# Performance work log

Measured on AMD Instinct MI355X. Metric: run time of the kernel, lower is better.

The kernel has to match this reference:

```python
import jax, jax.numpy as jnp
import numpy as np

# Config (matches init_kwargs): range [-32,32]^3, voxel 0.5 -> 128^3 grid; BEV 200x200
PC_LOW = np.array([-32.0, -32.0, -32.0], dtype=np.float32)
PC_HIGH = np.array([32.0, 32.0, 32.0], dtype=np.float32)
VOX = 0.5
G = 128
BEV_H, BEV_W = 200, 200
BN_EPS = 1e-5
STRIDES = [1, 2, 1, 2, 1, 1]


def setup_inputs() -> dict:
    key = jax.random.key(0)
    ks = jax.random.split(key, 10)
    N = 2_000_000
    xyz = jax.random.uniform(ks[0], (N, 3), jnp.float32, minval=-32.0, maxval=32.0)
    inten = jax.random.uniform(ks[1], (N, 1), jnp.float32)
    points = jnp.concatenate([xyz, inten], axis=1)  # (N,4)
    chans = [(32, 4), (64, 32), (64, 64), (128, 64), (128, 128), (256, 128)]
    inp = {"points": points}
    for i, (co, ci) in enumerate(chans):
        fan_in = ci * 27
        inp[f"w{i+1}"] = jax.random.normal(ks[2 + i], (co, ci, 3, 3, 3), jnp.float32) / np.sqrt(fan_in)
        inp[f"g{i+1}"] = jnp.ones((co,), jnp.float32)
        inp[f"b{i+1}"] = jnp.zeros((co,), jnp.float32)
    return inp


def _voxelize(points):
    # range filtering + floor-binning + clamp, faithful to voxelize_points (dense path: scatter-ADD)
    low = jnp.asarray(PC_LOW)
    high = jnp.asarray(PC_HIGH)
    mask = jnp.all((points[:, :3] >= low) & (points[:, :3] <= high), axis=1)
    coords = jnp.floor((points[:, :3] - low) / VOX).astype(jnp.int32)
    coords = jnp.clip(coords, 0, G - 1)
    vals = points * mask[:, None].astype(points.dtype)  # invalid points contribute 0
    # original indexes voxel_grid[:, z, y, x]
    grid = jnp.zeros((G, G, G, 4), points.dtype)
    grid = grid.at[coords[:, 2], coords[:, 1], coords[:, 0]].add(vals)
    return jnp.transpose(grid, (3, 0, 1, 2))  # (4, G, G, G)


def _conv3d(x, w, s):
    # PyTorch Conv3d(k=3, padding=1, stride=s), NCDHW
    return jax.lax.conv_general_dilated(
        x, w, window_strides=(s, s, s), padding=[(1, 1), (1, 1), (1, 1)],
        dimension_numbers=("NCDHW", "OIDHW", "NCDHW"))


def _bn_relu(x, g, b):
    # eval-mode BN: running_mean=0, running_var=1
    scale = (g / jnp.sqrt(1.0 + BN_EPS))[None, :, None, None, None]
    return jax.nn.relu(x * scale + b[None, :, None, None, None])


def reference(points, w1, w2, w3, w4, w5, w6,
              g1, g2, g3, g4, g5, g6,
              b1, b2, b3, b4, b5, b6):
    ws = [w1, w2, w3, w4, w5, w6]
    gs = [g1, g2, g3, g4, g5, g6]
    bs = [b1, b2, b3, b4, b5, b6]
    x = _voxelize(points)[None]  # (1,4,G,G,G)
    for w, g, b, s in zip(ws, gs, bs, STRIDES):
        x = _bn_relu(_conv3d(x, w, s), g, b)
    feat = x[0]  # (256, G/4, G/4, G/4)
    bev = jnp.max(feat, axis=2)  # torch.max(..., dim=2) on (C,D1,D2,D3) -> (C,D1,D3)
    # F.interpolate bilinear align_corners=False == jax.image.resize half-pixel bilinear
    bev = jax.image.resize(bev, (bev.shape[0], BEV_H, BEV_W), method="bilinear")
    return bev
```

## Files before the change

### kernel.cpp

```cpp
#include <hip/hip_runtime.h>
#include <hip/hip_fp16.h>
#include <cstdint>
#include <cstddef>

typedef __attribute__((ext_vector_type(8))) short short8;
typedef __attribute__((ext_vector_type(8))) _Float16 half8;
typedef __attribute__((ext_vector_type(16))) float f32x16;

__device__ __forceinline__ float bf2f(unsigned short u) { return __uint_as_float(((unsigned)u) << 16); }
__device__ __forceinline__ unsigned short f2bf(float f) {
    unsigned u = __float_as_uint(f);
    return (unsigned short)((u + 0x7fffu + ((u >> 16) & 1u)) >> 16);
}
__device__ __forceinline__ void sync_lds() {
    asm volatile("s_waitcnt lgkmcnt(0)\n\ts_barrier" ::: "memory");
}

static constexpr float BN_INV = 0.9999950000374997f;


__device__ __forceinline__ int vox_bucket(float4 p, bool& ok) {
    ok = !(p.x < -32.f || p.x > 32.f || p.y < -32.f || p.y > 32.f || p.z < -32.f || p.z > 32.f);
    int cy = min(max((int)floorf((p.y + 32.f) * 2.f), 0), 127);
    int cz = min(max((int)floorf((p.z + 32.f) * 2.f), 0), 127);
    return cz * 4 + (cy >> 5);
}

__global__ __launch_bounds__(256) void vox_count(const float4* __restrict__ pts,
                                                 int* __restrict__ cnt, int N) {
    __shared__ int h[512];
    for (int t = threadIdx.x; t < 512; t += 256) h[t] = 0;
    __syncthreads();
    int stride = gridDim.x * 256;
    for (int i = blockIdx.x * 256 + threadIdx.x; i < N; i += stride) {
        float4 p = pts[i];
        bool ok;
        int bk = vox_bucket(p, ok);
        if (ok) atomicAdd(&h[bk], 1);
    }
    __syncthreads();
    for (int t = threadIdx.x; t < 512; t += 256)
        if (h[t]) atomicAdd(&cnt[t], h[t]);
}

__global__ void vox_scan(const int* __restrict__ cnt, int* __restrict__ off,
                         int* __restrict__ cur) {
    __shared__ int c[512];
    int t = threadIdx.x;
    c[t] = cnt[t];
    __syncthreads();
    int s = 0;
    for (int i = 0; i < t; ++i) s += c[i];
    off[t] = s;
    cur[t] = s;
}

__global__ __launch_bounds__(256) void vox_scatter(const float4* __restrict__ pts,
                                                   int* __restrict__ cur,
                                                   float4* __restrict__ sorted, int N) {
    __shared__ int h[512];
    __shared__ int base[512];
    int b0 = blockIdx.x * 4096;
    for (int t = threadIdx.x; t < 512; t += 256) h[t] = 0;
    __syncthreads();
    float4 p[16];
    int bk[16];
#pragma unroll
    for (int j = 0; j < 16; ++j) {
        int i = b0 + j * 256 + threadIdx.x;
        bk[j] = -1;
        if (i < N) {
            p[j] = pts[i];
            bool ok;
            int b = vox_bucket(p[j], ok);
            if (ok) {
                bk[j] = b;
                atomicAdd(&h[b], 1);
            }
        }
    }
    __syncthreads();
    for (int t = threadIdx.x; t < 512; t += 256) {
        int n = h[t];
        base[t] = n ? atomicAdd(&cur[t], n) : 0;
        h[t] = 0;
    }
    __syncthreads();
#pragma unroll
    for (int j = 0; j < 16; ++j) {
        if (bk[j] >= 0) {
            int r = atomicAdd(&h[bk[j]], 1);
            sorted[base[bk[j]] + r] = p[j];
        }
    }
}

__global__ __launch_bounds__(256) void vox_accum(const float4* __restrict__ sorted,
                                                 const int* __restrict__ off,
                                                 const int* __restrict__ cnt,
                                                 __half2* __restrict__ grid) {
    __shared__ float s[32 * 128 * 4];
    for (int t = threadIdx.x; t < 16384; t += 256) s[t] = 0.f;
    __syncthreads();
    int bid = blockIdx.x;
    int bz = bid >> 2;
    int ylo = (bid & 3) << 5;
    int b = off[bid], n = cnt[bid];
    for (int i = threadIdx.x; i < n; i += 256) {
        float4 p = sorted[b + i];
        int cx = min(max((int)floorf((p.x + 32.f) * 2.f), 0), 127);
        int cy = min(max((int)floorf((p.y + 32.f) * 2.f), 0), 127);
        float* v = s + ((cy - ylo) * 128 + cx) * 4;
        unsafeAtomicAdd(v + 0, p.x);
        unsafeAtomicAdd(v + 1, p.y);
        unsafeAtomicAdd(v + 2, p.z);
        unsafeAtomicAdd(v + 3, p.w);
    }
    __syncthreads();
    for (int t = threadIdx.x; t < 4096; t += 256) {
        int ry = t >> 7, cx = t & 127;
        const float* v = s + t * 4;
        union { __half2 h[2]; float2 f; } u;
        u.h[0] = __floats2half2_rn(v[0], v[1]);
        u.h[1] = __floats2half2_rn(v[2], v[3]);
        int gi = (((bz + 1) * 130 + (ylo + ry + 1)) * 130 + (cx + 1)) * 2;
        *(float2*)(grid + gi) = u.f;
    }
}

__global__ __launch_bounds__(256) void pad_zero(unsigned short* __restrict__ buf,
                                                int Xp, int Zp, int C) {
    const int cpc = (C >= 8) ? (C / 8) : 1;
    long i = (long)blockIdx.x * 256 + threadIdx.x;
    long nz = (long)2 * Xp * Xp;
    long ny = (long)(Zp - 2) * 2 * Xp;
    long nx = (long)(Zp - 2) * (Xp - 2) * 2;
    long total = (nz + ny + nx) * cpc;
    if (i >= total) return;
    long cell = i / cpc;
    int ch = (int)(i - cell * cpc) * 8;
    int z, y, x;
    if (cell < nz) {
        long r = cell;
        z = (r >= (long)Xp * Xp) ? (Zp - 1) : 0;
        r %= (long)Xp * Xp;
        y = (int)(r / Xp);
        x = (int)(r % Xp);
    } else if (cell < nz + ny) {
        long r = cell - nz;
        z = 1 + (int)(r / (2 * Xp));
        int s = (int)(r % (2 * Xp));
        y = (s >= Xp) ? (Xp - 1) : 0;
        x = (s >= Xp) ? (s - Xp) : s;
    } else {
        long r = cell - nz - ny;
        z = 1 + (int)(r / ((Xp - 2) * 2));
        int s = (int)(r % ((Xp - 2) * 2));
        y = 1 + (s >> 1);
        x = (s & 1) ? (Xp - 1) : 0;
    }
    unsigned short* p = buf + (((long)z * Xp + y) * Xp + x) * C + ch;
    if (C >= 8) {
        *(short8*)p = (short8){0, 0, 0, 0, 0, 0, 0, 0};
    } else {
        *(float2*)p = (float2){0.f, 0.f};
    }
}
static inline int pad_blocks(int Xp, int Zp, int C) {
    long cells = (long)2 * Xp * Xp + (long)(Zp - 2) * 2 * Xp + (long)(Zp - 2) * (Xp - 2) * 2;
    long thr = cells * ((C >= 8) ? (C / 8) : 1);
    return (int)((thr + 255) / 256);
}

__global__ __launch_bounds__(256) void repack_w(const float* __restrict__ w, const float* __restrict__ g,
                                                unsigned short* __restrict__ o, int Co, int CI) {
    int i = blockIdx.x * 256 + threadIdx.x;
    int total = 27 * Co * CI;
    if (i >= total) return;
    int ci = i % CI;
    int t = i / CI;
    int co = t % Co;
    int k = t / Co;
    float v = w[((size_t)(co * CI + ci)) * 27 + k] * g[co] * BN_INV;
    o[i] = f2bf(v);
}
__global__ __launch_bounds__(256) void repack_w1m(const float* __restrict__ w, const float* __restrict__ g,
                                                  unsigned short* __restrict__ o) {
    int i = blockIdx.x * 256 + threadIdx.x;
    if (i >= 9 * 32 * 16) return;
    int k16 = i & 15;
    int co = (i >> 4) & 31;
    int p = i >> 9;
    float v = 0.f;
    if (k16 < 12) {
        int dx = k16 >> 2, ci = k16 & 3;
        int dz = p / 3, dy = p % 3;
        v = w[(co * 4 + ci) * 27 + dz * 9 + dy * 3 + dx] * g[co] * BN_INV;
    }
    o[i] = __half_as_ushort(__float2half(v));
}

__global__ __launch_bounds__(256) void conv1_mfma(
    const unsigned short* __restrict__ in, const unsigned short* __restrict__ wa,
    const float* __restrict__ beta, unsigned short* __restrict__ out,
    int zstart, int r0) {
    const int tid = threadIdx.x;
    const int l31 = tid & 31;
    const int lh = (tid >> 5) & 1;
    const int wv = tid >> 6;
    int v = blockIdx.x * 128 + wv * 32 + l31;
    int x = v & 127;
    int y = (v >> 7) & 127;
    int z = zstart + (v >> 14);

    const unsigned short* base = in + ((z * 130 + y) * 130 + x) * 4 + lh * 8;
    uint2 d0[9], d1[9];
    half8 a[9];
#pragma unroll
    for (int p = 0; p < 9; ++p) {
        int dz = p / 3, dy = p % 3;
        const unsigned short* rp = base + (dz * 130 + dy) * 520;
        d0[p] = *(const uint2*)(rp);
        d1[p] = *(const uint2*)(rp + 4);
        a[p] = *(const half8*)(wa + (p * 32 + l31) * 16 + lh * 8);
    }
    f32x16 acc = {0.f};
#pragma unroll
    for (int p = 0; p < 9; ++p) {
        uint4 braw = {d0[p].x, d0[p].y, d1[p].x, d1[p].y};
        half8 b = *(half8*)&braw;
        acc = __builtin_amdgcn_mfma_f32_32x32x16_f16(a[p], b, acc, 0, 0, 0);
    }
    int r = z - zstart + r0;
    int ob = ((r * 130 + (y + 1)) * 130 + (x + 1)) * 32;
#pragma unroll
    for (int g = 0; g < 4; ++g) {
        int cb = 4 * lh + 8 * g;
        float4 bt = *(const float4*)(beta + cb);
        ushort4 u;
        u.x = f2bf(fmaxf(acc[g * 4 + 0] + bt.x, 0.f));
        u.y = f2bf(fmaxf(acc[g * 4 + 1] + bt.y, 0.f));
        u.z = f2bf(fmaxf(acc[g * 4 + 2] + bt.z, 0.f));
        u.w = f2bf(fmaxf(acc[g * 4 + 3] + bt.w, 0.f));
        *(ushort4*)(out + ob + cb) = u;
    }
}

template <int CI, int KC, int S>
__global__ __launch_bounds__(256) void conv_mfma(
    const unsigned short* __restrict__ in, const unsigned short* __restrict__ wb,
    const float* __restrict__ beta, unsigned short* __restrict__ out,
    int D, int lgD, int Xp, int Xpo, int Co, int zin_base, int v_off) {

    constexpr int KCp = KC + 8;
    constexpr int OPB = KC / 8;
    constexpr int NB = KC / 16;
    constexpr int NA = KC / 32;
    constexpr int NCH = KC / 16;
    constexpr int NCC = CI / KC;
    constexpr int STOT = 27 * NCC;

    __shared__ __align__(16) short sA[2 * 64 * KCp];
    __shared__ __align__(16) short sB[2 * 128 * KCp];

    const int tid = threadIdx.x;
    const int l31 = tid & 31;
    const int lh = (tid >> 5) & 1;
    const int wv = tid >> 6;

    const unsigned gx = gridDim.x;
    const unsigned lin = blockIdx.y * gx + blockIdx.x;
    const unsigned q = (gx * gridDim.y) >> 3;
    const unsigned lin2 = (lin & 7) * q + (lin >> 3);
    const unsigned bxs = lin2 % gx;
    const unsigned bys = lin2 / gx;
    const int co0 = bxs * 64;

    int bgIdx[NB], blB[NB];
#pragma unroll
    for (int j = 0; j < NB; ++j) {
        int idx = tid + j * 256;
        int vL = idx / OPB;
        int oct = idx - vL * OPB;
        int vg = v_off + bys * 128 + vL;
        int x = vg & (D - 1);
        int ry = vg >> lgD;
        int y = ry & (D - 1);
        int z = ry >> lgD;
        bgIdx[j] = ((z * S * Xp + y * S) * Xp + x * S) * CI + oct * 8;
        blB[j] = vL * KCp + oct * 8;
    }
    int agIdx[NA], alA[NA];
#pragma unroll
    for (int j = 0; j < NA; ++j) {
        int idx = tid + j * 256;
        int cA = idx / OPB;
        int oct = idx - cA * OPB;
        agIdx[j] = (co0 + cA) * CI + oct * 8;
        alA[j] = cA * KCp + oct * 8;
    }
    const int bfr = (wv * 32 + l31) * KCp + lh * 8;
    const int afr = l31 * KCp + lh * 8;

    short8 rB[2][NB], rA[2][NA];

    auto loadStage = [&](int s, int r) {
        int k = s / NCC;
        int c0 = (s - k * NCC) * KC;
        int dz = k / 9;
        int rr = k - dz * 9;
        int dy = rr / 3;
        int dx = rr - dy * 3;
        int kb = (((dz - zin_base) * Xp + dy) * Xp + dx) * CI + c0;
        int ka = k * Co * CI + c0;
#pragma unroll
        for (int j = 0; j < NB; ++j) rB[r][j] = *(const short8*)(in + bgIdx[j] + kb);
#pragma unroll
        for (int j = 0; j < NA; ++j) rA[r][j] = *(const short8*)(wb + agIdx[j] + ka);
    };
    auto storeLDS = [&](int r, int buf) {
#pragma unroll
        for (int j = 0; j < NB; ++j) *(short8*)(sB + buf * 128 * KCp + blB[j]) = rB[r][j];
#pragma unroll
        for (int j = 0; j < NA; ++j) *(short8*)(sA + buf * 64 * KCp + alA[j]) = rA[r][j];
    };

    f32x16 acc0 = {0.f}, acc1 = {0.f};

    loadStage(0, 0);
    loadStage(1, 1);
    storeLDS(0, 0);
    sync_lds();

#pragma unroll
    for (int s = 0; s < STOT; ++s) {
        if (s + 2 < STOT) loadStage(s + 2, s & 1);
        const short* pB = sB + (s & 1) * 128 * KCp + bfr;
        const short* pA = sA + (s & 1) * 64 * KCp + afr;
#pragma unroll
        for (int c = 0; c < NCH; ++c) {
            short8 bv = *(const short8*)(pB + c * 16);
            short8 a0 = *(const short8*)(pA + c * 16);
            short8 a1 = *(const short8*)(pA + 32 * KCp + c * 16);
            acc0 = __builtin_amdgcn_mfma_f32_32x32x16_bf16(a0, bv, acc0, 0, 0, 0);
            acc1 = __builtin_amdgcn_mfma_f32_32x32x16_bf16(a1, bv, acc1, 0, 0, 0);
        }
        if (s + 1 < STOT) {
            storeLDS((s + 1) & 1, (s + 1) & 1);
            sync_lds();
        }
    }

    int vg = v_off + bys * 128 + wv * 32 + l31;
    int x = vg & (D - 1);
    int ry = vg >> lgD;
    int y = ry & (D - 1);
    int z = ry >> lgD;
    size_t ob = (((size_t)(z + 1) * Xpo + (y + 1)) * Xpo + (x + 1)) * Co + co0;
#pragma unroll
    for (int cot = 0; cot < 2; ++cot) {
        const f32x16& a = cot ? acc1 : acc0;
#pragma unroll
        for (int g = 0; g < 4; ++g) {
            int cb = cot * 32 + 4 * lh + 8 * g;
            float4 bt = *(const float4*)(beta + co0 + cb);
            ushort4 u;
            u.x = f2bf(fmaxf(a[g * 4 + 0] + bt.x, 0.f));
            u.y = f2bf(fmaxf(a[g * 4 + 1] + bt.y, 0.f));
            u.z = f2bf(fmaxf(a[g * 4 + 2] + bt.z, 0.f));
            u.w = f2bf(fmaxf(a[g * 4 + 3] + bt.w, 0.f));
            *(ushort4*)(out + ob + cb) = u;
        }
    }
}

template <int CI, int S>
__global__ __launch_bounds__(256, 2) void conv_mfma_w(
    const unsigned short* __restrict__ in, const unsigned short* __restrict__ wb,
    const float* __restrict__ beta, unsigned short* __restrict__ out,
    int D, int lgD, int Xp, int Xpo, int Co, int zin_base, int v_off) {

    constexpr int KC = 64;
    constexpr int KCp = KC + 8;
    constexpr int OPB = KC / 8;
    constexpr int NB = 4;
    constexpr int NA = 4;
    constexpr int NCH = 4;
    constexpr int NCC = CI / KC;
    constexpr int STOT = 27 * NCC;

    __shared__ __align__(16) short sA[2 * 128 * KCp];
    __shared__ __align__(16) short sB[2 * 128 * KCp];

    const int tid = threadIdx.x;
    const int l31 = tid & 31;
    const int lh = (tid >> 5) & 1;
    const int wv = tid >> 6;
    const int wr = wv >> 1;
    const int wc = wv & 1;

    const unsigned gx = gridDim.x;
    const unsigned lin = blockIdx.y * gx + blockIdx.x;
    const unsigned q = (gx * gridDim.y) >> 3;
    const unsigned lin2 = (lin & 7) * q + (lin >> 3);
    const unsigned bxs = lin2 % gx;
    const unsigned bys = lin2 / gx;
    const int co0 = bxs * 128;

    int bgIdx[NB], blB[NB];
#pragma unroll
    for (int j = 0; j < NB; ++j) {
        int idx = tid + j * 256;
        int vL = idx / OPB;
        int oct = idx - vL * OPB;
        int vg = v_off + bys * 128 + vL;
        int x = vg & (D - 1);
        int ry = vg >> lgD;
        int y = ry & (D - 1);
        int z = ry >> lgD;
        bgIdx[j] = ((z * S * Xp + y * S) * Xp + x * S) * CI + oct * 8;
        blB[j] = vL * KCp + oct * 8;
    }
    int agIdx[NA], alA[NA];
#pragma unroll
    for (int j = 0; j < NA; ++j) {
        int idx = tid + j * 256;
        int cA = idx / OPB;
        int oct = idx - cA * OPB;
        agIdx[j] = (co0 + cA) * CI + oct * 8;
        alA[j] = cA * KCp + oct * 8;
    }
    const int bfr = (wc * 64 + l31) * KCp + lh * 8;
    const int afr = (wr * 64 + l31) * KCp + lh * 8;

    short8 rB[2][NB], rA[2][NA];

    auto loadStage = [&](int s, int r) {
        int k = s / NCC;
        int c0 = (s - k * NCC) * KC;
        int dz = k / 9;
        int rr = k - dz * 9;
        int dy = rr / 3;
        int dx = rr - dy * 3;
        int kb = (((dz - zin_base) * Xp + dy) * Xp + dx) * CI + c0;
        int ka = k * Co * CI + c0;
#pragma unroll
        for (int j = 0; j < NB; ++j) rB[r][j] = *(const short8*)(in + bgIdx[j] + kb);
#pragma unroll
        for (int j = 0; j < NA; ++j) rA[r][j] = *(const short8*)(wb + agIdx[j] + ka);
    };
    auto storeLDS = [&](int r, int buf) {
#pragma unroll
        for (int j = 0; j < NB; ++j) *(short8*)(sB + buf * 128 * KCp + blB[j]) = rB[r][j];
#pragma unroll
        for (int j = 0; j < NA; ++j) *(short8*)(sA + buf * 128 * KCp + alA[j]) = rA[r][j];
    };

    f32x16 acc00 = {0.f}, acc01 = {0.f}, acc10 = {0.f}, acc11 = {0.f};

    loadStage(0, 0);
    loadStage(1, 1);
    storeLDS(0, 0);
    sync_lds();

#pragma unroll
    for (int s = 0; s < STOT; ++s) {
        if (s + 2 < STOT) loadStage(s + 2, s & 1);
        const short* pB = sB + (s & 1) * 128 * KCp + bfr;
        const short* pA = sA + (s & 1) * 128 * KCp + afr;
#pragma unroll
        for (int c = 0; c < NCH; ++c) {
            short8 b0 = *(const short8*)(pB + c * 16);
            short8 b1 = *(const short8*)(pB + 32 * KCp + c * 16);
            short8 a0 = *(const short8*)(pA + c * 16);
            short8 a1 = *(const short8*)(pA + 32 * KCp + c * 16);
            acc00 = __builtin_amdgcn_mfma_f32_32x32x16_bf16(a0, b0, acc00, 0, 0, 0);
            acc01 = __builtin_amdgcn_mfma_f32_32x32x16_bf16(a0, b1, acc01, 0, 0, 0);
            acc10 = __builtin_amdgcn_mfma_f32_32x32x16_bf16(a1, b0, acc10, 0, 0, 0);
            acc11 = __builtin_amdgcn_mfma_f32_32x32x16_bf16(a1, b1, acc11, 0, 0, 0);
        }
        if (s + 1 < STOT) {
            storeLDS((s + 1) & 1, (s + 1) & 1);
            sync_lds();
        }
    }

#pragma unroll
    for (int i = 0; i < 2; ++i) {
#pragma unroll
        for (int j = 0; j < 2; ++j) {
            const f32x16& a = (i == 0) ? (j == 0 ? acc00 : acc01) : (j == 0 ? acc10 : acc11);
            int vg2 = v_off + bys * 128 + wc * 64 + j * 32 + l31;
            int x = vg2 & (D - 1);
            int ry = vg2 >> lgD;
            int y = ry & (D - 1);
            int z = ry >> lgD;
            int cbase = co0 + wr * 64 + i * 32;
            size_t ob = (((size_t)(z + 1) * Xpo + (y + 1)) * Xpo + (x + 1)) * Co + cbase;
#pragma unroll
            for (int g = 0; g < 4; ++g) {
                int cb = 4 * lh + 8 * g;
                float4 bt = *(const float4*)(beta + cbase + cb);
                ushort4 u;
                u.x = f2bf(fmaxf(a[g * 4 + 0] + bt.x, 0.f));
                u.y = f2bf(fmaxf(a[g * 4 + 1] + bt.y, 0.f));
                u.z = f2bf(fmaxf(a[g * 4 + 2] + bt.z, 0.f));
                u.w = f2bf(fmaxf(a[g * 4 + 3] + bt.w, 0.f));
                *(ushort4*)(out + ob + cb) = u;
            }
        }
    }
}

__global__ __launch_bounds__(256) void bev_max_kernel(const unsigned short* __restrict__ feat,
                                                      float* __restrict__ bev) {
    int z = blockIdx.x >> 5;
    int x = blockIdx.x & 31;
    int c = threadIdx.x;
    const unsigned short* p = feat + ((((z + 1) * 34) + 1) * 34 + (x + 1)) * 256 + c;
    float mx = 0.f;
#pragma unroll
    for (int y = 0; y < 32; ++y) mx = fmaxf(mx, bf2f(p[y * 34 * 256]));
    bev[(z * 32 + x) * 256 + c] = mx;
}

__global__ __launch_bounds__(256) void resize_kernel(const float* __restrict__ bev,
                                                     float* __restrict__ out) {
    int i = blockIdx.x * 256 + threadIdx.x;
    if (i >= 256 * 200 * 200) return;
    int ox = i % 200;
    int t = i / 200;
    int oy = t % 200;
    int c = t / 200;
    const float sc = 32.0f / 200.0f;
    float fy = (oy + 0.5f) * sc - 0.5f;
    float fx = (ox + 0.5f) * sc - 0.5f;
    float fy0 = floorf(fy), fx0 = floorf(fx);
    float ty = fy - fy0, tx = fx - fx0;
    int y0 = min(max((int)fy0, 0), 31), y1 = min(max((int)fy0 + 1, 0), 31);
    int x0 = min(max((int)fx0, 0), 31), x1 = min(max((int)fx0 + 1, 0), 31);
    float v00 = bev[(y0 * 32 + x0) * 256 + c], v01 = bev[(y0 * 32 + x1) * 256 + c];
    float v10 = bev[(y1 * 32 + x0) * 256 + c], v11 = bev[(y1 * 32 + x1) * 256 + c];
    float top = v00 + tx * (v01 - v00);
    float bot = v10 + tx * (v11 - v10);
    out[i] = top + ty * (bot - top);
}

extern "C" void kernel_launch(void* const* d_in, const int* in_sizes, int n_in,
                              void* d_out, int out_size, void* d_ws, size_t ws_size,
                              hipStream_t stream) {
    const float* points = (const float*)d_in[0];
    int N = in_sizes[0] / 4;
    const float *W[6], *G[6], *B[6];
    for (int i = 0; i < 6; ++i) {
        W[i] = (const float*)d_in[1 + 3 * i];
        G[i] = (const float*)d_in[2 + 3 * i];
        B[i] = (const float*)d_in[3 + 3 * i];
    }

    char* ws = (char*)d_ws;
    const size_t MiB = 1ull << 20;
    unsigned short* gridH = (unsigned short*)(ws);
    int* cnt = (int*)(ws + 17580032);
    int* off = cnt + 512;
    int* cur = off + 512;
    float4* sorted = (float4*)(ws + 18 * MiB);
    unsigned short* O1s = (unsigned short*)(ws + 18 * MiB);
    unsigned short* O2p = (unsigned short*)(ws + 104 * MiB);
    unsigned short* O3p = (unsigned short*)(ws);
    unsigned short* O4p = (unsigned short*)(ws + 37 * MiB);
    unsigned short* O5p = (unsigned short*)(ws + 48 * MiB);
    unsigned short* O6p = (unsigned short*)(ws + 59 * MiB);
    float* bev = (float*)(ws + 80 * MiB);
    unsigned short* wc1 = (unsigned short*)(ws + 140 * MiB);
    unsigned short* wb2 = (unsigned short*)(ws + 140 * MiB + 16384);
    unsigned short* wb3 = wb2 + 27 * 64 * 32;
    unsigned short* wb4 = wb3 + 27 * 64 * 64;
    unsigned short* wb5 = wb4 + 27 * 128 * 64;
    unsigned short* wb6 = wb5 + 27 * 128 * 128;

    repack_w1m<<<18, 256, 0, stream>>>(W[0], G[0], wc1);
    repack_w<<<216, 256, 0, stream>>>(W[1], G[1], wb2, 64, 32);
    repack_w<<<432, 256, 0, stream>>>(W[2], G[2], wb3, 64, 64);
    repack_w<<<864, 256, 0, stream>>>(W[3], G[3], wb4, 128, 64);
    repack_w<<<1728, 256, 0, stream>>>(W[4], G[4], wb5, 128, 128);
    repack_w<<<3456, 256, 0, stream>>>(W[5], G[5], wb6, 256, 128);

    pad_zero<<<pad_blocks(130, 130, 4), 256, 0, stream>>>(gridH, 130, 130, 4);
    hipMemsetAsync(cnt, 0, 2048, stream);
    pad_zero<<<pad_blocks(66, 66, 64), 256, 0, stream>>>(O2p, 66, 66, 64);
    vox_count<<<1024, 256, 0, stream>>>((const float4*)points, cnt, N);
    vox_scan<<<1, 512, 0, stream>>>(cnt, off, cur);
    vox_scatter<<<(N + 4095) / 4096, 256, 0, stream>>>((const float4*)points, cur, sorted, N);
    vox_accum<<<512, 256, 0, stream>>>(sorted, off, cnt, (__half2*)gridH);

    pad_zero<<<pad_blocks(130, 65, 32), 256, 0, stream>>>(O1s, 130, 65, 32);
    conv1_mfma<<<8192, 256, 0, stream>>>(gridH, wc1, B[0], O1s, 0, 1);
    conv_mfma<32, 32, 2><<<dim3(1, 1024), 256, 0, stream>>>(O1s, wb2, B[1], O2p, 64, 6, 130, 66, 64, 0, 0);
    conv1_mfma<<<8320, 256, 0, stream>>>(gridH, wc1, B[0], O1s, 63, 0);
    conv_mfma<32, 32, 2><<<dim3(1, 1024), 256, 0, stream>>>(O1s, wb2, B[1], O2p, 64, 6, 130, 66, 64, 64, 131072);

    pad_zero<<<pad_blocks(66, 66, 64), 256, 0, stream>>>(O3p, 66, 66, 64);
    pad_zero<<<pad_blocks(34, 34, 128), 256, 0, stream>>>(O4p, 34, 34, 128);
    pad_zero<<<pad_blocks(34, 34, 128), 256, 0, stream>>>(O5p, 34, 34, 128);
    pad_zero<<<pad_blocks(34, 34, 256), 256, 0, stream>>>(O6p, 34, 34, 256);

    conv_mfma<64, 64, 1><<<dim3(1, 2048), 256, 0, stream>>>(O2p, wb3, B[2], O3p, 64, 6, 66, 66, 64, 0, 0);
    conv_mfma_w<64, 2><<<dim3(1, 256), 256, 0, stream>>>(O3p, wb4, B[3], O4p, 32, 5, 66, 34, 128, 0, 0);
    conv_mfma_w<128, 1><<<dim3(1, 256), 256, 0, stream>>>(O4p, wb5, B[4], O5p, 32, 5, 34, 34, 128, 0, 0);
    conv_mfma_w<128, 1><<<dim3(2, 256), 256, 0, stream>>>(O5p, wb6, B[5], O6p, 32, 5, 34, 34, 256, 0, 0);

    bev_max_kernel<<<1024, 256, 0, stream>>>(O6p, bev);
    resize_kernel<<<40000, 256, 0, stream>>>(bev, (float*)d_out);
}
```

Measured before the change: 628.8 us.

## Enlarge conv2/conv3 tiles to 256 voxels with 2x2 MFMA register blocking

Replaces the generic conv_mfma kernel used for layers 2 and 3 with conv_mfma_p. Each block now covers 256 output voxels by 64 channels, and each wave computes a 2x2 grid of 32x32 MFMA tiles, so every LDS fragment is reused twice and fewer blocks are launched. The K chunk is fixed at 32, LDS rows are paired into 72-element padded rows to reduce bank conflicts, and launch bounds request 3 blocks per SM. The cost is more accumulator registers, and for conv3 the stage loop is only partially unrolled, giving more stages per weight load.

```diff
diff --git a/kernel.cpp b/kernel.cpp
--- a/kernel.cpp
+++ b/kernel.cpp
@@ -246,22 +246,19 @@
     }
 }
 
-template <int CI, int KC, int S>
-__global__ __launch_bounds__(256) void conv_mfma(
+template <int CI, int S>
+__global__ __launch_bounds__(256, 3) void conv_mfma_p(
     const unsigned short* __restrict__ in, const unsigned short* __restrict__ wb,
     const float* __restrict__ beta, unsigned short* __restrict__ out,
     int D, int lgD, int Xp, int Xpo, int Co, int zin_base, int v_off) {
 
-    constexpr int KCp = KC + 8;
-    constexpr int OPB = KC / 8;
-    constexpr int NB = KC / 16;
-    constexpr int NA = KC / 32;
-    constexpr int NCH = KC / 16;
+    constexpr int KC = 32;
     constexpr int NCC = CI / KC;
     constexpr int STOT = 27 * NCC;
-
-    __shared__ __align__(16) short sA[2 * 64 * KCp];
-    __shared__ __align__(16) short sB[2 * 128 * KCp];
+    constexpr int PR = 72;
+
+    __shared__ __align__(16) short sB[2 * 128 * PR];
+    __shared__ __align__(16) short sA[2 * 32 * PR];
 
     const int tid = threadIdx.x;
     const int l31 = tid & 31;
@@ -276,33 +273,33 @@
     const unsigned bys = lin2 / gx;
     const int co0 = bxs * 64;
 
-    int bgIdx[NB], blB[NB];
-#pragma unroll
-    for (int j = 0; j < NB; ++j) {
+    int bgIdx[4], blB[4];
+#pragma unroll
+    for (int j = 0; j < 4; ++j) {
         int idx = tid + j * 256;
-        int vL = idx / OPB;
-        int oct = idx - vL * OPB;
-        int vg = v_off + bys * 128 + vL;
+        int vL = idx >> 2;
+        int oct = idx & 3;
+        int vg = v_off + bys * 256 + vL;
         int x = vg & (D - 1);
         int ry = vg >> lgD;
         int y = ry & (D - 1);
         int z = ry >> lgD;
         bgIdx[j] = ((z * S * Xp + y * S) * Xp + x * S) * CI + oct * 8;
-        blB[j] = vL * KCp + oct * 8;
-    }
-    int agIdx[NA], alA[NA];
-#pragma unroll
-    for (int j = 0; j < NA; ++j) {
-        int idx = tid + j * 256;
-        int cA = idx / OPB;
-        int oct = idx - cA * OPB;
-        agIdx[j] = (co0 + cA) * CI + oct * 8;
-        alA[j] = cA * KCp + oct * 8;
-    }
-    const int bfr = (wv * 32 + l31) * KCp + lh * 8;
-    const int afr = l31 * KCp + lh * 8;
-
-    short8 rB[2][NB], rA[2][NA];
+        blB[j] = (vL >> 1) * PR + (vL & 1) * 32 + oct * 8;
+    }
+    const int cA = tid >> 2;
+    const int aoct = tid & 3;
+    const int agIdx = (co0 + cA) * CI + aoct * 8;
+    const int alA = (cA >> 1) * PR + (cA & 1) * 32 + aoct * 8;
+
+    const int vb0 = wv * 64 + l31;
+    const int vb1 = vb0 + 32;
+    const int bfr0 = (vb0 >> 1) * PR + (vb0 & 1) * 32 + lh * 8;
+    const int bfr1 = (vb1 >> 1) * PR + (vb1 & 1) * 32 + lh * 8;
+    const int afr0 = (l31 >> 1) * PR + (l31 & 1) * 32 + lh * 8;
+    const int afr1 = ((l31 + 32) >> 1) * PR + (l31 & 1) * 32 + lh * 8;
+
+    short8 rB[2][4], rA[2][1];
 
     auto loadStage = [&](int s, int r) {
         int k = s / NCC;
@@ -314,62 +311,73 @@
         int kb = (((dz - zin_base) * Xp + dy) * Xp + dx) * CI + c0;
         int ka = k * Co * CI + c0;
 #pragma unroll
-        for (int j = 0; j < NB; ++j) rB[r][j] = *(const short8*)(in + bgIdx[j] + kb);
-#pragma unroll
-        for (int j = 0; j < NA; ++j) rA[r][j] = *(const short8*)(wb + agIdx[j] + ka);
+        for (int j = 0; j < 4; ++j) rB[r][j] = *(const short8*)(in + bgIdx[j] + kb);
+        rA[r][0] = *(const short8*)(wb + agIdx + ka);
     };
     auto storeLDS = [&](int r, int buf) {
 #pragma unroll
-        for (int j = 0; j < NB; ++j) *(short8*)(sB + buf * 128 * KCp + blB[j]) = rB[r][j];
-#pragma unroll
-        for (int j = 0; j < NA; ++j) *(short8*)(sA + buf * 64 * KCp + alA[j]) = rA[r][j];
+        for (int j = 0; j < 4; ++j) *(short8*)(sB + buf * 128 * PR + blB[j]) = rB[r][j];
+        *(short8*)(sA + buf * 32 * PR + alA) = rA[r][0];
     };
 
-    f32x16 acc0 = {0.f}, acc1 = {0.f};
+    f32x16 acc00 = {0.f}, acc01 = {0.f}, acc10 = {0.f}, acc11 = {0.f};
 
     loadStage(0, 0);
     loadStage(1, 1);
     storeLDS(0, 0);
     sync_lds();
 
-#pragma unroll
-    for (int s = 0; s < STOT; ++s) {
+    auto stage = [&](int s) {
         if (s + 2 < STOT) loadStage(s + 2, s & 1);
-        const short* pB = sB + (s & 1) * 128 * KCp + bfr;
-        const short* pA = sA + (s & 1) * 64 * KCp + afr;
-#pragma unroll
-        for (int c = 0; c < NCH; ++c) {
-            short8 bv = *(const short8*)(pB + c * 16);
-            short8 a0 = *(const short8*)(pA + c * 16);
-            short8 a1 = *(const short8*)(pA + 32 * KCp + c * 16);
-            acc0 = __builtin_amdgcn_mfma_f32_32x32x16_bf16(a0, bv, acc0, 0, 0, 0);
-            acc1 = __builtin_amdgcn_mfma_f32_32x32x16_bf16(a1, bv, acc1, 0, 0, 0);
+        const short* pB = sB + (s & 1) * 128 * PR;
+        const short* pA = sA + (s & 1) * 32 * PR;
+#pragma unroll
+        for (int c = 0; c < 2; ++c) {
+            short8 a0 = *(const short8*)(pA + afr0 + c * 16);
+            short8 a1 = *(const short8*)(pA + afr1 + c * 16);
+            short8 b0 = *(const short8*)(pB + bfr0 + c * 16);
+            short8 b1 = *(const short8*)(pB + bfr1 + c * 16);
+            acc00 = __builtin_amdgcn_mfma_f32_32x32x16_bf16(a0, b0, acc00, 0, 0, 0);
+            acc01 = __builtin_amdgcn_mfma_f32_32x32x16_bf16(a0, b1, acc01, 0, 0, 0);
+            acc10 = __builtin_amdgcn_mfma_f32_32x32x16_bf16(a1, b0, acc10, 0, 0, 0);
+            acc11 = __builtin_amdgcn_mfma_f32_32x32x16_bf16(a1, b1, acc11, 0, 0, 0);
         }
         if (s + 1 < STOT) {
             storeLDS((s + 1) & 1, (s + 1) & 1);
             sync_lds();
         }
-    }
-
-    int vg = v_off + bys * 128 + wv * 32 + l31;
-    int x = vg & (D - 1);
-    int ry = vg >> lgD;
-    int y = ry & (D - 1);
-    int z = ry >> lgD;
-    size_t ob = (((size_t)(z + 1) * Xpo + (y + 1)) * Xpo + (x + 1)) * Co + co0;
-#pragma unroll
-    for (int cot = 0; cot < 2; ++cot) {
-        const f32x16& a = cot ? acc1 : acc0;
-#pragma unroll
-        for (int g = 0; g < 4; ++g) {
-            int cb = cot * 32 + 4 * lh + 8 * g;
-            float4 bt = *(const float4*)(beta + co0 + cb);
-            ushort4 u;
-            u.x = f2bf(fmaxf(a[g * 4 + 0] + bt.x, 0.f));
-            u.y = f2bf(fmaxf(a[g * 4 + 1] + bt.y, 0.f));
-            u.z = f2bf(fmaxf(a[g * 4 + 2] + bt.z, 0.f));
-            u.w = f2bf(fmaxf(a[g * 4 + 3] + bt.w, 0.f));
-            *(ushort4*)(out + ob + cb) = u;
+    };
+    if constexpr (STOT <= 32) {
+#pragma unroll
+        for (int s = 0; s < STOT; ++s) stage(s);
+    } else {
+#pragma unroll 2
+        for (int s = 0; s < STOT; ++s) stage(s);
+    }
+
+#pragma unroll
+    for (int i = 0; i < 2; ++i) {
+#pragma unroll
+        for (int j = 0; j < 2; ++j) {
+            const f32x16& a = (i == 0) ? (j == 0 ? acc00 : acc01) : (j == 0 ? acc10 : acc11);
+            int vg2 = v_off + bys * 256 + wv * 64 + j * 32 + l31;
+            int x = vg2 & (D - 1);
+            int ry = vg2 >> lgD;
+            int y = ry & (D - 1);
+            int z = ry >> lgD;
+            int cbase = co0 + i * 32;
+            size_t ob = (((size_t)(z + 1) * Xpo + (y + 1)) * Xpo + (x + 1)) * Co + cbase;
+#pragma unroll
+            for (int g = 0; g < 4; ++g) {
+                int cb = 4 * lh + 8 * g;
+                float4 bt = *(const float4*)(beta + cbase + cb);
+                ushort4 u;
+                u.x = f2bf(fmaxf(a[g * 4 + 0] + bt.x, 0.f));
+                u.y = f2bf(fmaxf(a[g * 4 + 1] + bt.y, 0.f));
+                u.z = f2bf(fmaxf(a[g * 4 + 2] + bt.z, 0.f));
+                u.w = f2bf(fmaxf(a[g * 4 + 3] + bt.w, 0.f));
+                *(ushort4*)(out + ob + cb) = u;
+            }
         }
     }
 }
@@ -596,16 +604,16 @@
 
     pad_zero<<<pad_blocks(130, 65, 32), 256, 0, stream>>>(O1s, 130, 65, 32);
     conv1_mfma<<<8192, 256, 0, stream>>>(gridH, wc1, B[0], O1s, 0, 1);
-    conv_mfma<32, 32, 2><<<dim3(1, 1024), 256, 0, stream>>>(O1s, wb2, B[1], O2p, 64, 6, 130, 66, 64, 0, 0);
+    conv_mfma_p<32, 2><<<dim3(1, 512), 256, 0, stream>>>(O1s, wb2, B[1], O2p, 64, 6, 130, 66, 64, 0, 0);
     conv1_mfma<<<8320, 256, 0, stream>>>(gridH, wc1, B[0], O1s, 63, 0);
-    conv_mfma<32, 32, 2><<<dim3(1, 1024), 256, 0, stream>>>(O1s, wb2, B[1], O2p, 64, 6, 130, 66, 64, 64, 131072);
+    conv_mfma_p<32, 2><<<dim3(1, 512), 256, 0, stream>>>(O1s, wb2, B[1], O2p, 64, 6, 130, 66, 64, 64, 131072);
 
     pad_zero<<<pad_blocks(66, 66, 64), 256, 0, stream>>>(O3p, 66, 66, 64);
     pad_zero<<<pad_blocks(34, 34, 128), 256, 0, stream>>>(O4p, 34, 34, 128);
     pad_zero<<<pad_blocks(34, 34, 128), 256, 0, stream>>>(O5p, 34, 34, 128);
     pad_zero<<<pad_blocks(34, 34, 256), 256, 0, stream>>>(O6p, 34, 34, 256);
 
-    conv_mfma<64, 64, 1><<<dim3(1, 2048), 256, 0, stream>>>(O2p, wb3, B[2], O3p, 64, 6, 66, 66, 64, 0, 0);
+    conv_mfma_p<64, 1><<<dim3(1, 1024), 256, 0, stream>>>(O2p, wb3, B[2], O3p, 64, 6, 66, 66, 64, 0, 0);
     conv_mfma_w<64, 2><<<dim3(1, 256), 256, 0, stream>>>(O3p, wb4, B[3], O4p, 32, 5, 66, 34, 128, 0, 0);
     conv_mfma_w<128, 1><<<dim3(1, 256), 256, 0, stream>>>(O4p, wb5, B[4], O5p, 32, 5, 34, 34, 128, 0, 0);
     conv_mfma_w<128, 1><<<dim3(2, 256), 256, 0, stream>>>(O5p, wb6, B[5], O6p, 32, 5, 34, 34, 256, 0, 0);
```

Result: slower. 642.7 us (+2.2%).
